# Performance work log

Measured on AMD Instinct MI355X. Metric: run time of the kernel, lower is better.

The kernel has to match this reference:

```python
import jax, jax.numpy as jnp
import numpy as np

DIM = 192; HEADS = 6; WS = 7; RES = 56; SHIFT = 3
HEAD_DIM = DIM // HEADS
SCALE = HEAD_DIM ** -0.5
N = WS * WS
EPS = 1e-5

def _rel_pos_index():
    coords = np.stack(np.meshgrid(np.arange(WS), np.arange(WS), indexing='ij')).reshape(2, -1)
    rel = coords[:, :, None] - coords[:, None, :]  # [2,N,N]
    rel = rel.transpose(1, 2, 0)
    rel[:, :, 0] += WS - 1
    rel[:, :, 1] += WS - 1
    rel[:, :, 0] *= 2 * WS - 1
    return rel.sum(-1)  # [N,N]

def _attn_mask():
    img = np.zeros((RES, RES), dtype=np.float32)
    slices = (slice(0, -WS), slice(-WS, -SHIFT), slice(-SHIFT, None))
    cnt = 0
    for h in slices:
        for w in slices:
            img[h, w] = cnt; cnt += 1
    mw = img.reshape(RES // WS, WS, RES // WS, WS).transpose(0, 2, 1, 3).reshape(-1, N)  # [nW,N]
    diff = mw[:, None, :] - mw[:, :, None]
    return np.where(diff != 0, -100.0, 0.0).astype(np.float32)  # [nW,N,N]

REL_IDX = jnp.asarray(_rel_pos_index())
ATTN_MASK = jnp.asarray(_attn_mask())

def _ln(x, g, b):
    mu = x.mean(-1, keepdims=True)
    var = ((x - mu) ** 2).mean(-1, keepdims=True)
    return (x - mu) * jax.lax.rsqrt(var + EPS) * g + b

def setup_inputs() -> dict:
    key = jax.random.key(0)
    ks = jax.random.split(key, 8)
    d = {
        'x': jax.random.normal(ks[0], (32, RES * RES, DIM), jnp.float32),
        'norm1_g': jnp.ones((DIM,), jnp.float32), 'norm1_b': jnp.zeros((DIM,), jnp.float32),
        'qkv_w': jax.random.normal(ks[1], (DIM, 3 * DIM), jnp.float32) * 0.02,
        'qkv_b': jnp.zeros((3 * DIM,), jnp.float32),
        'proj_w': jax.random.normal(ks[2], (DIM, DIM), jnp.float32) * 0.02,
        'proj_b': jnp.zeros((DIM,), jnp.float32),
        'bias_table': jax.random.normal(ks[3], ((2 * WS - 1) ** 2, HEADS), jnp.float32) * 0.02,
        'norm2_g': jnp.ones((DIM,), jnp.float32), 'norm2_b': jnp.zeros((DIM,), jnp.float32),
        'fc1_w': jax.random.normal(ks[4], (DIM, 4 * DIM), jnp.float32) * 0.02,
        'fc1_b': jnp.zeros((4 * DIM,), jnp.float32),
        'fc2_w': jax.random.normal(ks[5], (4 * DIM, DIM), jnp.float32) * 0.02,
        'fc2_b': jnp.zeros((DIM,), jnp.float32),
    }
    return d

def reference(x, norm1_g, norm1_b, qkv_w, qkv_b, proj_w, proj_b, bias_table,
              norm2_g, norm2_b, fc1_w, fc1_b, fc2_w, fc2_b):
    B, L, C = x.shape
    H = W = RES
    shortcut = x
    h = _ln(x, norm1_g, norm1_b).reshape(B, H, W, C)
    # cyclic shift
    h = jnp.roll(h, (-SHIFT, -SHIFT), axis=(1, 2))
    # window partition -> [B*nW, N, C]
    nH = H // WS
    h = h.reshape(B, nH, WS, nH, WS, C).transpose(0, 1, 3, 2, 4, 5).reshape(-1, N, C)
    BW = h.shape[0]
    # windowed MHSA
    qkv = (h @ qkv_w + qkv_b).reshape(BW, N, 3, HEADS, HEAD_DIM)
    q, k, v = qkv[:, :, 0], qkv[:, :, 1], qkv[:, :, 2]  # [BW,N,h,hd]
    attn = jnp.einsum('bnhd,bmhd->bhnm', q, k) * SCALE  # [BW,h,N,N]
    bias = bias_table[REL_IDX.reshape(-1)].reshape(N, N, HEADS).transpose(2, 0, 1)
    attn = attn + bias[None]
    nW = ATTN_MASK.shape[0]
    attn = attn.reshape(BW // nW, nW, HEADS, N, N) + ATTN_MASK[None, :, None]
    attn = jax.nn.softmax(attn.reshape(BW, HEADS, N, N), axis=-1)
    h = jnp.einsum('bhnm,bmhd->bnhd', attn, v).reshape(BW, N, C)
    h = h @ proj_w + proj_b
    # window reverse
    h = h.reshape(B, nH, nH, WS, WS, C).transpose(0, 1, 3, 2, 4, 5).reshape(B, H, W, C)
    h = jnp.roll(h, (SHIFT, SHIFT), axis=(1, 2)).reshape(B, L, C)
    x = shortcut + h
    # MLP
    m = _ln(x, norm2_g, norm2_b)
    m = jax.nn.gelu(m @ fc1_w + fc1_b, approximate=False) @ fc2_w + fc2_b
    return x + m
```

## Files before the change

kernel.cpp:

```cpp
#include <hip/hip_runtime.h>
#include <hip/hip_bf16.h>
#include <math.h>

typedef __attribute__((ext_vector_type(8))) short bh8;
typedef __attribute__((ext_vector_type(4))) short sh4;
typedef __attribute__((ext_vector_type(4))) float fx4;

__device__ __forceinline__ fx4 mfma_bf16(bh8 a, bh8 b, fx4 c) {
    return __builtin_amdgcn_mfma_f32_16x16x32_bf16(a, b, c, 0, 0, 0);
}

__device__ __forceinline__ void gload16(const __hip_bfloat16* g, __hip_bfloat16* l) {
    __builtin_amdgcn_global_load_lds(
        (const __attribute__((address_space(1))) void*)g,
        (__attribute__((address_space(3))) void*)l,
        16, 0, 0);
}

__device__ __forceinline__ float fast_erf(float u) {
    float au = fabsf(u);
    float t  = __builtin_amdgcn_rcpf(1.0f + 0.3275911f * au);
    float p  = ((((1.061405429f * t - 1.453152027f) * t + 1.421413741f) * t
                 - 0.284496736f) * t + 0.254829592f) * t;
    float e  = __expf(-u * u);
    return copysignf(1.0f - p * e, u);
}

#define WAITV6 do { asm volatile("s_waitcnt vmcnt(6)" ::: "memory"); \
                    __builtin_amdgcn_sched_barrier(0); } while (0)
#define WAITV0 do { asm volatile("s_waitcnt vmcnt(0)" ::: "memory"); \
                    __builtin_amdgcn_sched_barrier(0); } while (0)
#define LGKM0  do { asm volatile("s_waitcnt lgkmcnt(0)" ::: "memory"); \
                    __builtin_amdgcn_sched_barrier(0); } while (0)
#define BARR   do { __builtin_amdgcn_s_barrier(); \
                    __builtin_amdgcn_sched_barrier(0); } while (0)

__global__ __launch_bounds__(256)
void convw_all_k(const float* __restrict__ qkv_w, const float* __restrict__ proj_w,
                 const float* __restrict__ fc1_w, const float* __restrict__ fc2_w,
                 __hip_bfloat16* __restrict__ wq, __hip_bfloat16* __restrict__ wp,
                 __hip_bfloat16* __restrict__ w1, __hip_bfloat16* __restrict__ w2)
{
    int idx = blockIdx.x * 256 + threadIdx.x;
    if (idx < 110592) {
        int k = idx / 576, n = idx - k * 576;
        wq[(size_t)n * 192 + k] = __float2bfloat16(qkv_w[idx]);
        return;
    }
    idx -= 110592;
    if (idx < 36864) {
        int k = idx / 192, n = idx - k * 192;
        wp[(size_t)n * 192 + k] = __float2bfloat16(proj_w[idx]);
        return;
    }
    idx -= 36864;
    if (idx < 147456) {
        int k = idx / 768, n = idx - k * 768;
        w1[(size_t)n * 192 + k] = __float2bfloat16(fc1_w[idx]);
        return;
    }
    idx -= 147456;
    if (idx < 147456) {
        int k = idx / 192, n = idx - k * 192;
        w2[(size_t)n * 768 + k] = __float2bfloat16(fc2_w[idx]);
    }
}

__global__ __launch_bounds__(256)
void ln1_gather_k(const float* __restrict__ x, const float* __restrict__ g,
                  const float* __restrict__ bia, __hip_bfloat16* __restrict__ xw)
{
    const int wave = threadIdx.x >> 6, lane = threadIdx.x & 63;
    const int t = blockIdx.x * 4 + wave;
    const int w = t / 49, n = t - w * 49;
    const int b = w >> 6, wrem = w & 63, wi = wrem >> 3, wj = wrem & 7;
    const int i = n / 7, j = n - i * 7;
    int sr = wi * 7 + i + 3; if (sr >= 56) sr -= 56;
    int sc = wj * 7 + j + 3; if (sc >= 56) sc -= 56;
    const float* xp = x + ((size_t)b * 3136 + sr * 56 + sc) * 192;
    float v0 = xp[lane], v1 = xp[lane + 64], v2 = xp[lane + 128];
    float s = v0 + v1 + v2;
    float q = v0 * v0 + v1 * v1 + v2 * v2;
    for (int off = 32; off > 0; off >>= 1) {
        s += __shfl_down(s, off, 64);
        q += __shfl_down(q, off, 64);
    }
    s = __shfl(s, 0, 64); q = __shfl(q, 0, 64);
    float mean = s * (1.0f / 192.0f);
    float var  = q * (1.0f / 192.0f) - mean * mean;
    float rstd = rsqrtf(var + 1e-5f);
    __hip_bfloat16* op = xw + (size_t)t * 192;
    op[lane]       = __float2bfloat16((v0 - mean) * rstd * g[lane]       + bia[lane]);
    op[lane + 64]  = __float2bfloat16((v1 - mean) * rstd * g[lane + 64]  + bia[lane + 64]);
    op[lane + 128] = __float2bfloat16((v2 - mean) * rstd * g[lane + 128] + bia[lane + 128]);
}

template<int K, int NOUT>
__global__ __launch_bounds__(256)
void gemm_qkv_k(const __hip_bfloat16* __restrict__ A,
                const __hip_bfloat16* __restrict__ Bt,
                const float* __restrict__ bias,
                __hip_bfloat16* __restrict__ outv)
{
    __shared__ __align__(16) __hip_bfloat16 As[128 * 32];
    __shared__ __align__(16) __hip_bfloat16 Bs[64 * 32];
    const int tid  = threadIdx.x;
    const int lane = tid & 63, wave = tid >> 6;
    const int quad = lane >> 4, l15 = lane & 15;

    const int nb = NOUT / 64;
    const int wk = (blockIdx.x & 7) * ((int)gridDim.x >> 3) + ((int)blockIdx.x >> 3);
    const int m0 = (wk / nb) * 128, n0 = (wk % nb) * 64;

    const int arow = lane >> 2, acol = (lane & 3) * 8;
    const __hip_bfloat16* Ag0 = A  + (size_t)(m0 + wave * 32 + arow)      * K + acol;
    const __hip_bfloat16* Ag1 = A  + (size_t)(m0 + wave * 32 + 16 + arow) * K + acol;
    const __hip_bfloat16* Bg  = Bt + (size_t)(n0 + wave * 16 + arow)      * K + acol;
    __hip_bfloat16* Al0 = &As[(wave * 32)      * 32];
    __hip_bfloat16* Al1 = &As[(wave * 32 + 16) * 32];
    __hip_bfloat16* Bl  = &Bs[(wave * 16)      * 32];

    fx4 acc[2][4];
#pragma unroll
    for (int mi = 0; mi < 2; mi++)
#pragma unroll
        for (int ni = 0; ni < 4; ni++) acc[mi][ni] = {0.f, 0.f, 0.f, 0.f};

    for (int k0 = 0; k0 < K; k0 += 32) {
        gload16(Ag0 + k0, Al0);
        gload16(Ag1 + k0, Al1);
        gload16(Bg  + k0, Bl);
        __syncthreads();
        bh8 a0 = *(const bh8*)&As[(wave * 32 + l15)      * 32 + quad * 8];
        bh8 a1 = *(const bh8*)&As[(wave * 32 + 16 + l15) * 32 + quad * 8];
        bh8 b0 = *(const bh8*)&Bs[(0 * 16 + l15) * 32 + quad * 8];
        bh8 b1 = *(const bh8*)&Bs[(1 * 16 + l15) * 32 + quad * 8];
        bh8 b2 = *(const bh8*)&Bs[(2 * 16 + l15) * 32 + quad * 8];
        bh8 b3 = *(const bh8*)&Bs[(3 * 16 + l15) * 32 + quad * 8];
        acc[0][0] = mfma_bf16(a0, b0, acc[0][0]);
        acc[0][1] = mfma_bf16(a0, b1, acc[0][1]);
        acc[0][2] = mfma_bf16(a0, b2, acc[0][2]);
        acc[0][3] = mfma_bf16(a0, b3, acc[0][3]);
        acc[1][0] = mfma_bf16(a1, b0, acc[1][0]);
        acc[1][1] = mfma_bf16(a1, b1, acc[1][1]);
        acc[1][2] = mfma_bf16(a1, b2, acc[1][2]);
        acc[1][3] = mfma_bf16(a1, b3, acc[1][3]);
        __syncthreads();
    }

#pragma unroll
    for (int mi = 0; mi < 2; mi++)
#pragma unroll
    for (int ni = 0; ni < 4; ni++) {
        const int n = n0 + ni * 16 + l15;
        const float bn = bias[n];
#pragma unroll
        for (int r = 0; r < 4; r++) {
            const int m = m0 + wave * 32 + mi * 16 + quad * 4 + r;
            float v = acc[mi][ni][r] + bn;
            if (n < 192) v *= 0.17677669529663687f;
            outv[(size_t)m * NOUT + n] = __float2bfloat16(v);
        }
    }
}

__global__ __launch_bounds__(256, 2)
void mlp_k(const __hip_bfloat16* __restrict__ A,
           const __hip_bfloat16* __restrict__ W1t,
           const __hip_bfloat16* __restrict__ W2t,
           const float* __restrict__ b1,
           const float* __restrict__ b2,
           float* __restrict__ out)
{
    __shared__ __align__(16) __hip_bfloat16 W1s[2][6][32][32];
    __shared__ __align__(16) __hip_bfloat16 W2s[2][192][32];
    __shared__ __align__(16) __hip_bfloat16 Hs[128][40];
    __shared__ __align__(16) float b1s[768];

    const int tid  = threadIdx.x;
    const int lane = tid & 63, wave = tid >> 6;
    const int quad = lane >> 4, l15 = lane & 15;
    const int m0 = blockIdx.x * 128;
    const int arow = lane >> 2, acol = (lane & 3) * 8;

    if (tid < 192) ((fx4*)b1s)[tid] = ((const fx4*)b1)[tid];
    LGKM0;

    bh8 xr[2][6];
    const __hip_bfloat16* xg = A + (size_t)(m0 + wave * 32 + l15) * 192 + quad * 8;
#pragma unroll
    for (int rt = 0; rt < 2; rt++)
#pragma unroll
        for (int kc = 0; kc < 6; kc++)
            xr[rt][kc] = *(const bh8*)(xg + rt * 16 * 192 + kc * 32);

    auto stage = [&](int bf, int c) {
#pragma unroll
        for (int i = 0; i < 3; i++) {
            const int g = wave * 3 + i;
            const int kc = g >> 1, half = g & 1;
            gload16(W1t + (size_t)(c * 32 + half * 16 + arow) * 192 + kc * 32 + acol,
                    &W1s[bf][kc][half * 16][0]);
            gload16(W2t + (size_t)(g * 16 + arow) * 768 + c * 32 + acol,
                    &W2s[bf][g * 16][0]);
        }
    };

    fx4 acc2[2][12];
#pragma unroll
    for (int rt = 0; rt < 2; rt++)
#pragma unroll
        for (int nt = 0; nt < 12; nt++) acc2[rt][nt] = {0.f, 0.f, 0.f, 0.f};

    stage(0, 0);
    stage(1, 1);

    int cur = 0;
    for (int c = 0; c < 23; ++c) {
        WAITV6;
        BARR;

        fx4 bv0 = *(const fx4*)&b1s[c * 32 + quad * 4];
        fx4 bv1 = *(const fx4*)&b1s[c * 32 + 16 + quad * 4];

        fx4 acc1[2][2];
        acc1[0][0] = {0.f, 0.f, 0.f, 0.f}; acc1[0][1] = {0.f, 0.f, 0.f, 0.f};
        acc1[1][0] = {0.f, 0.f, 0.f, 0.f}; acc1[1][1] = {0.f, 0.f, 0.f, 0.f};
        __builtin_amdgcn_s_setprio(1);
#pragma unroll
        for (int kc = 0; kc < 6; kc++) {
#pragma unroll
            for (int ni = 0; ni < 2; ni++) {
                bh8 w = *(const bh8*)&W1s[cur][kc][ni * 16 + l15][quad * 8];
                acc1[0][ni] = mfma_bf16(w, xr[0][kc], acc1[0][ni]);
                acc1[1][ni] = mfma_bf16(w, xr[1][kc], acc1[1][ni]);
            }
        }
        __builtin_amdgcn_s_setprio(0);

#pragma unroll
        for (int rt = 0; rt < 2; rt++) {
#pragma unroll
            for (int ni = 0; ni < 2; ni++) {
                const fx4 bv = ni ? bv1 : bv0;
                sh4 pk;
#pragma unroll
                for (int r = 0; r < 4; r++) {
                    float v = acc1[rt][ni][r] + bv[r];
                    float h = 0.5f * v * (1.0f + fast_erf(v * 0.70710678118654752f));
                    union { __hip_bfloat16 hb; short s; } u;
                    u.hb = __float2bfloat16(h);
                    pk[r] = u.s;
                }
                *(sh4*)&Hs[wave * 32 + rt * 16 + l15][ni * 16 + quad * 4] = pk;
            }
        }
        LGKM0;

        bh8 ha0 = *(const bh8*)&Hs[wave * 32 + l15][quad * 8];
        bh8 ha1 = *(const bh8*)&Hs[wave * 32 + 16 + l15][quad * 8];
        __builtin_amdgcn_s_setprio(1);
#pragma unroll
        for (int nt = 0; nt < 12; nt++) {
            bh8 w2 = *(const bh8*)&W2s[cur][nt * 16 + l15][quad * 8];
            acc2[0][nt] = mfma_bf16(ha0, w2, acc2[0][nt]);
            acc2[1][nt] = mfma_bf16(ha1, w2, acc2[1][nt]);
        }
        __builtin_amdgcn_s_setprio(0);

        BARR;
        if (c < 22) stage(cur, c + 2);
        cur ^= 1;
    }

    {
        WAITV0;
        BARR;
        fx4 bv0 = *(const fx4*)&b1s[23 * 32 + 0 * 16 + quad * 4];
        fx4 bv1 = *(const fx4*)&b1s[23 * 32 + 1 * 16 + quad * 4];
        fx4 acc1[2][2];
        acc1[0][0] = {0.f, 0.f, 0.f, 0.f}; acc1[0][1] = {0.f, 0.f, 0.f, 0.f};
        acc1[1][0] = {0.f, 0.f, 0.f, 0.f}; acc1[1][1] = {0.f, 0.f, 0.f, 0.f};
#pragma unroll
        for (int kc = 0; kc < 6; kc++) {
#pragma unroll
            for (int ni = 0; ni < 2; ni++) {
                bh8 w = *(const bh8*)&W1s[cur][kc][ni * 16 + l15][quad * 8];
                acc1[0][ni] = mfma_bf16(w, xr[0][kc], acc1[0][ni]);
                acc1[1][ni] = mfma_bf16(w, xr[1][kc], acc1[1][ni]);
            }
        }
#pragma unroll
        for (int rt = 0; rt < 2; rt++) {
#pragma unroll
            for (int ni = 0; ni < 2; ni++) {
                const fx4 bv = ni ? bv1 : bv0;
                sh4 pk;
#pragma unroll
                for (int r = 0; r < 4; r++) {
                    float v = acc1[rt][ni][r] + bv[r];
                    float h = 0.5f * v * (1.0f + fast_erf(v * 0.70710678118654752f));
                    union { __hip_bfloat16 hb; short s; } u;
                    u.hb = __float2bfloat16(h);
                    pk[r] = u.s;
                }
                *(sh4*)&Hs[wave * 32 + rt * 16 + l15][ni * 16 + quad * 4] = pk;
            }
        }
        LGKM0;
        bh8 ha0 = *(const bh8*)&Hs[wave * 32 + l15][quad * 8];
        bh8 ha1 = *(const bh8*)&Hs[wave * 32 + 16 + l15][quad * 8];
#pragma unroll
        for (int nt = 0; nt < 12; nt++) {
            bh8 w2 = *(const bh8*)&W2s[cur][nt * 16 + l15][quad * 8];
            acc2[0][nt] = mfma_bf16(ha0, w2, acc2[0][nt]);
            acc2[1][nt] = mfma_bf16(ha1, w2, acc2[1][nt]);
        }
    }

#pragma unroll
    for (int rt = 0; rt < 2; rt++)
#pragma unroll
    for (int nt = 0; nt < 12; nt++) {
        const int n = nt * 16 + l15;
        const float bn = b2[n];
#pragma unroll
        for (int r = 0; r < 4; r++) {
            const int m = m0 + wave * 32 + rt * 16 + quad * 4 + r;
            out[(size_t)m * 192 + n] += acc2[rt][nt][r] + bn;
        }
    }
}

__global__ __launch_bounds__(256)
void projln_k(const __hip_bfloat16* __restrict__ A,
              const __hip_bfloat16* __restrict__ Bt,
              const float* __restrict__ pb,
              const float* __restrict__ xresid,
              const float* __restrict__ g2,
              const float* __restrict__ b2,
              float* __restrict__ x1out,
              __hip_bfloat16* __restrict__ y2out)
{
    __shared__ __align__(16) __hip_bfloat16 As[64 * 32];
    __shared__ __align__(16) __hip_bfloat16 Bs[192 * 32];
    const int tid  = threadIdx.x;
    const int lane = tid & 63, wave = tid >> 6;
    const int quad = lane >> 4, l15 = lane & 15;
    const int m0 = blockIdx.x * 64;

    const int arow = lane >> 2, acol = (lane & 3) * 8;
    const __hip_bfloat16* Ag = A + (size_t)(m0 + wave * 16 + arow) * 192 + acol;
    __hip_bfloat16* Al = &As[(wave * 16) * 32];
    const __hip_bfloat16* Bg0 = Bt + (size_t)((wave + 0) * 16 + arow) * 192 + acol;
    const __hip_bfloat16* Bg1 = Bt + (size_t)((wave + 4) * 16 + arow) * 192 + acol;
    const __hip_bfloat16* Bg2 = Bt + (size_t)((wave + 8) * 16 + arow) * 192 + acol;
    __hip_bfloat16* Bl0 = &Bs[((wave + 0) * 16) * 32];
    __hip_bfloat16* Bl1 = &Bs[((wave + 4) * 16) * 32];
    __hip_bfloat16* Bl2 = &Bs[((wave + 8) * 16) * 32];

    fx4 acc[12];
#pragma unroll
    for (int ct = 0; ct < 12; ct++) acc[ct] = {0.f, 0.f, 0.f, 0.f};

    for (int k0 = 0; k0 < 192; k0 += 32) {
        gload16(Ag  + k0, Al);
        gload16(Bg0 + k0, Bl0);
        gload16(Bg1 + k0, Bl1);
        gload16(Bg2 + k0, Bl2);
        __syncthreads();
        bh8 a = *(const bh8*)&As[(wave * 16 + l15) * 32 + quad * 8];
#pragma unroll
        for (int ct = 0; ct < 12; ct++) {
            bh8 b = *(const bh8*)&Bs[(ct * 16 + l15) * 32 + quad * 8];
            acc[ct] = mfma_bf16(a, b, acc[ct]);
        }
        __syncthreads();
    }

#pragma unroll
    for (int r = 0; r < 4; r++) {
        const int row = m0 + wave * 16 + quad * 4 + r;
        float vv[12];
        float s = 0.f, q = 0.f;
#pragma unroll
        for (int ct = 0; ct < 12; ct++) {
            const int col = ct * 16 + l15;
            float v = acc[ct][r] + pb[col] + xresid[(size_t)row * 192 + col];
            vv[ct] = v;
            x1out[(size_t)row * 192 + col] = v;
            s += v;
            q += v * v;
        }
        s += __shfl_xor(s, 1, 64);  q += __shfl_xor(q, 1, 64);
        s += __shfl_xor(s, 2, 64);  q += __shfl_xor(q, 2, 64);
        s += __shfl_xor(s, 4, 64);  q += __shfl_xor(q, 4, 64);
        s += __shfl_xor(s, 8, 64);  q += __shfl_xor(q, 8, 64);
        float mean = s * (1.0f / 192.0f);
        float var  = q * (1.0f / 192.0f) - mean * mean;
        float rstd = rsqrtf(var + 1e-5f);
#pragma unroll
        for (int ct = 0; ct < 12; ct++) {
            const int col = ct * 16 + l15;
            float y = (vv[ct] - mean) * rstd * g2[col] + b2[col];
            y2out[(size_t)row * 192 + col] = __float2bfloat16(y);
        }
    }
}

__global__ __launch_bounds__(256)
void attn_k(const __hip_bfloat16* __restrict__ qkv,
            const float* __restrict__ bias_table,
            __hip_bfloat16* __restrict__ aout)
{
    __shared__ __align__(16) __hip_bfloat16 Qb[64 * 32];
    __shared__ __align__(16) __hip_bfloat16 Kb[64 * 32];
    __shared__ __align__(16) __hip_bfloat16 Vt[32 * 72];
    __shared__ __align__(16) __hip_bfloat16 Ps[64 * 72];
    __shared__ float bias_h[169];

    const int tid  = threadIdx.x;
    const int lane = tid & 63, wave = tid >> 6;
    const int quad = lane >> 4, l15 = lane & 15;
    const int wk = (blockIdx.x & 7) * 1536 + ((int)blockIdx.x >> 3);
    const int w = wk / 6, hd = wk % 6;
    const int b = w >> 6, wrem = w & 63, wi = wrem >> 3, wj = wrem & 7;
    const size_t base = (size_t)w * 49 * 576 + hd * 32;

    if (tid < 169) bias_h[tid] = bias_table[tid * 6 + hd];

    bh8 z = {0, 0, 0, 0, 0, 0, 0, 0};
    {
        int row = tid >> 2, ch = (tid & 3) * 8;
        if (row < 49) {
            *(bh8*)&Qb[row * 32 + ch] = *(const bh8*)(qkv + base + (size_t)row * 576 + ch);
            *(bh8*)&Kb[row * 32 + ch] = *(const bh8*)(qkv + base + (size_t)row * 576 + 192 + ch);
        } else {
            *(bh8*)&Qb[row * 32 + ch] = z;
            *(bh8*)&Kb[row * 32 + ch] = z;
        }
        for (int i = tid; i < 288; i += 256)
            *(bh8*)&Vt[i * 8] = z;
    }
    __syncthreads();
    for (int idx = tid; idx < 49 * 32; idx += 256) {
        int n = idx >> 5, d = idx & 31;
        Vt[d * 72 + n] = qkv[base + (size_t)n * 576 + 384 + d];
    }
    __syncthreads();

    fx4 zf = {0.f, 0.f, 0.f, 0.f};
    bh8 aq = *(const bh8*)&Qb[(wave * 16 + l15) * 32 + quad * 8];
    fx4 sarr[4];
#pragma unroll
    for (int ni = 0; ni < 4; ni++) {
        bh8 bk = *(const bh8*)&Kb[(ni * 16 + l15) * 32 + quad * 8];
        sarr[ni] = mfma_bf16(aq, bk, zf);
    }

    int iarr[4], ria[4], cia[4], mbi[4];
#pragma unroll
    for (int r = 0; r < 4; r++) {
        int i = wave * 16 + quad * 4 + r;
        int ri = i / 7, ci = i - ri * 7;
        iarr[r] = i; ria[r] = ri; cia[r] = ci;
        int ar = wi * 7 + ri, ac = wj * 7 + ci;
        int br = (ar < 49) ? 0 : ((ar < 53) ? 1 : 2);
        int bc = (ac < 49) ? 0 : ((ac < 53) ? 1 : 2);
        mbi[r] = br * 3 + bc;
    }
    float vals[4][4];
#pragma unroll
    for (int ni = 0; ni < 4; ni++) {
        int jcol = ni * 16 + l15;
        int rj = jcol / 7, cj = jcol - rj * 7;
        int ar = wi * 7 + rj, ac = wj * 7 + cj;
        int br = (ar < 49) ? 0 : ((ar < 53) ? 1 : 2);
        int bc = (ac < 49) ? 0 : ((ac < 53) ? 1 : 2);
        int mbj = br * 3 + bc;
#pragma unroll
        for (int r = 0; r < 4; r++) {
            float v;
            if (jcol >= 49)            v = -1e30f;
            else if (iarr[r] >= 49)    v = 0.0f;
            else {
                int bidx = (ria[r] - rj + 6) * 13 + (cia[r] - cj + 6);
                v = sarr[ni][r] + bias_h[bidx] + ((mbi[r] != mbj) ? -100.0f : 0.0f);
            }
            vals[ni][r] = v;
        }
    }
#pragma unroll
    for (int r = 0; r < 4; r++) {
        float mx = fmaxf(fmaxf(vals[0][r], vals[1][r]), fmaxf(vals[2][r], vals[3][r]));
        mx = fmaxf(mx, __shfl_xor(mx, 1, 64));
        mx = fmaxf(mx, __shfl_xor(mx, 2, 64));
        mx = fmaxf(mx, __shfl_xor(mx, 4, 64));
        mx = fmaxf(mx, __shfl_xor(mx, 8, 64));
        float e0 = __expf(vals[0][r] - mx);
        float e1 = __expf(vals[1][r] - mx);
        float e2 = __expf(vals[2][r] - mx);
        float e3 = __expf(vals[3][r] - mx);
        float sm = e0 + e1 + e2 + e3;
        sm += __shfl_xor(sm, 1, 64);
        sm += __shfl_xor(sm, 2, 64);
        sm += __shfl_xor(sm, 4, 64);
        sm += __shfl_xor(sm, 8, 64);
        float inv = 1.0f / sm;
        int prow = (wave * 16 + quad * 4 + r) * 72;
        Ps[prow + 0 * 16 + l15] = __float2bfloat16(e0 * inv);
        Ps[prow + 1 * 16 + l15] = __float2bfloat16(e1 * inv);
        Ps[prow + 2 * 16 + l15] = __float2bfloat16(e2 * inv);
        Ps[prow + 3 * 16 + l15] = __float2bfloat16(e3 * inv);
    }
    __syncthreads();

    fx4 o0 = zf, o1 = zf;
#pragma unroll
    for (int k0 = 0; k0 < 64; k0 += 32) {
        bh8 ap  = *(const bh8*)&Ps[(wave * 16 + l15) * 72 + k0 + quad * 8];
        bh8 bv0 = *(const bh8*)&Vt[(l15)      * 72 + k0 + quad * 8];
        bh8 bv1 = *(const bh8*)&Vt[(16 + l15) * 72 + k0 + quad * 8];
        o0 = mfma_bf16(ap, bv0, o0);
        o1 = mfma_bf16(ap, bv1, o1);
    }

#pragma unroll
    for (int r = 0; r < 4; r++) {
        int m = wave * 16 + quad * 4 + r;
        if (m < 49) {
            int i = m / 7, j2 = m - i * 7;
            int orow = wi * 7 + i + 3;  if (orow >= 56) orow -= 56;
            int ocol = wj * 7 + j2 + 3; if (ocol >= 56) ocol -= 56;
            size_t t = (size_t)b * 3136 + orow * 56 + ocol;
            aout[t * 192 + hd * 32 + l15]      = __float2bfloat16(o0[r]);
            aout[t * 192 + hd * 32 + 16 + l15] = __float2bfloat16(o1[r]);
        }
    }
}

extern "C" void kernel_launch(void* const* d_in, const int* in_sizes, int n_in,
                              void* d_out, int out_size, void* d_ws, size_t ws_size,
                              hipStream_t stream)
{
    const float* x      = (const float*)d_in[0];
    const float* n1g    = (const float*)d_in[1];
    const float* n1b    = (const float*)d_in[2];
    const float* qkv_w  = (const float*)d_in[3];
    const float* qkv_b  = (const float*)d_in[4];
    const float* proj_w = (const float*)d_in[5];
    const float* proj_b = (const float*)d_in[6];
    const float* btab   = (const float*)d_in[7];
    const float* n2g    = (const float*)d_in[8];
    const float* n2b    = (const float*)d_in[9];
    const float* fc1_w  = (const float*)d_in[10];
    const float* fc1_b  = (const float*)d_in[11];
    const float* fc2_w  = (const float*)d_in[12];
    const float* fc2_b  = (const float*)d_in[13];

    char* ws = (char*)d_ws;
    __hip_bfloat16* buf1    = (__hip_bfloat16*)(ws + 0);
    __hip_bfloat16* buf2    = (__hip_bfloat16*)(ws + 38535168);
    __hip_bfloat16* wt_qkv  = (__hip_bfloat16*)(ws + 192675840);
    __hip_bfloat16* wt_proj = (__hip_bfloat16*)(ws + 192897024);
    __hip_bfloat16* wt_fc1  = (__hip_bfloat16*)(ws + 192970752);
    __hip_bfloat16* wt_fc2  = (__hip_bfloat16*)(ws + 193265664);
    float*          x1      = (float*)d_out;

    convw_all_k<<<dim3(1728), 256, 0, stream>>>(qkv_w, proj_w, fc1_w, fc2_w,
                                                wt_qkv, wt_proj, wt_fc1, wt_fc2);

    ln1_gather_k<<<dim3(25088), 256, 0, stream>>>(x, n1g, n1b, buf1);

    gemm_qkv_k<192, 576><<<dim3(7056), 256, 0, stream>>>(buf1, wt_qkv, qkv_b, buf2);

    attn_k<<<dim3(12288), 256, 0, stream>>>(buf2, btab, buf1);

    projln_k<<<dim3(1568), 256, 0, stream>>>(buf1, wt_proj, proj_b, x, n2g, n2b, x1, buf1);

    mlp_k<<<dim3(784), 256, 0, stream>>>(buf1, wt_fc1, wt_fc2, fc1_b, fc2_b, x1);
}
```

Before: 444.2 us.

## Fuse LayerNorm1 and window gather into the QKV GEMM kernel

Merges the LN1+shift/window-gather kernel with the QKV projection GEMM. Each block normalizes 64 tokens into LDS as bf16, then loops over all 9 output column tiles reusing that A tile. This removes the bf16 intermediate write/read of the normalized activations and one kernel launch. The cost is a smaller M tile per block and serialized N tiles with barriers, which may reduce parallelism and weight reuse per block.

```diff
diff --git a/kernel.cpp b/kernel.cpp
--- a/kernel.cpp
+++ b/kernel.cpp
@@ -24,6 +24,12 @@
                  - 0.284496736f) * t + 0.254829592f) * t;
     float e  = __expf(-u * u);
     return copysignf(1.0f - p * e, u);
+}
+
+__device__ __forceinline__ short bf16s(float f) {
+    union { __hip_bfloat16 h; short s; } u;
+    u.h = __float2bfloat16(f);
+    return u.s;
 }
 
 #define WAITV6 do { asm volatile("s_waitcnt vmcnt(6)" ::: "memory"); \
@@ -67,100 +73,97 @@
 }
 
 __global__ __launch_bounds__(256)
-void ln1_gather_k(const float* __restrict__ x, const float* __restrict__ g,
-                  const float* __restrict__ bia, __hip_bfloat16* __restrict__ xw)
+void lnqkv_k(const float* __restrict__ x, const float* __restrict__ g,
+             const float* __restrict__ bia,
+             const __hip_bfloat16* __restrict__ Bt,
+             const float* __restrict__ qb,
+             __hip_bfloat16* __restrict__ outv)
 {
-    const int wave = threadIdx.x >> 6, lane = threadIdx.x & 63;
-    const int t = blockIdx.x * 4 + wave;
-    const int w = t / 49, n = t - w * 49;
-    const int b = w >> 6, wrem = w & 63, wi = wrem >> 3, wj = wrem & 7;
-    const int i = n / 7, j = n - i * 7;
-    int sr = wi * 7 + i + 3; if (sr >= 56) sr -= 56;
-    int sc = wj * 7 + j + 3; if (sc >= 56) sc -= 56;
-    const float* xp = x + ((size_t)b * 3136 + sr * 56 + sc) * 192;
-    float v0 = xp[lane], v1 = xp[lane + 64], v2 = xp[lane + 128];
-    float s = v0 + v1 + v2;
-    float q = v0 * v0 + v1 * v1 + v2 * v2;
-    for (int off = 32; off > 0; off >>= 1) {
-        s += __shfl_down(s, off, 64);
-        q += __shfl_down(q, off, 64);
-    }
-    s = __shfl(s, 0, 64); q = __shfl(q, 0, 64);
-    float mean = s * (1.0f / 192.0f);
-    float var  = q * (1.0f / 192.0f) - mean * mean;
-    float rstd = rsqrtf(var + 1e-5f);
-    __hip_bfloat16* op = xw + (size_t)t * 192;
-    op[lane]       = __float2bfloat16((v0 - mean) * rstd * g[lane]       + bia[lane]);
-    op[lane + 64]  = __float2bfloat16((v1 - mean) * rstd * g[lane + 64]  + bia[lane + 64]);
-    op[lane + 128] = __float2bfloat16((v2 - mean) * rstd * g[lane + 128] + bia[lane + 128]);
-}
-
-template<int K, int NOUT>
-__global__ __launch_bounds__(256)
-void gemm_qkv_k(const __hip_bfloat16* __restrict__ A,
-                const __hip_bfloat16* __restrict__ Bt,
-                const float* __restrict__ bias,
-                __hip_bfloat16* __restrict__ outv)
-{
-    __shared__ __align__(16) __hip_bfloat16 As[128 * 32];
-    __shared__ __align__(16) __hip_bfloat16 Bs[64 * 32];
+    __shared__ __align__(16) __hip_bfloat16 Xs[6][64][32];
+    __shared__ __align__(16) __hip_bfloat16 Bs[6][64][32];
+
     const int tid  = threadIdx.x;
     const int lane = tid & 63, wave = tid >> 6;
     const int quad = lane >> 4, l15 = lane & 15;
-
-    const int nb = NOUT / 64;
-    const int wk = (blockIdx.x & 7) * ((int)gridDim.x >> 3) + ((int)blockIdx.x >> 3);
-    const int m0 = (wk / nb) * 128, n0 = (wk % nb) * 64;
-
+    const int m0 = blockIdx.x * 64;
     const int arow = lane >> 2, acol = (lane & 3) * 8;
-    const __hip_bfloat16* Ag0 = A  + (size_t)(m0 + wave * 32 + arow)      * K + acol;
-    const __hip_bfloat16* Ag1 = A  + (size_t)(m0 + wave * 32 + 16 + arow) * K + acol;
-    const __hip_bfloat16* Bg  = Bt + (size_t)(n0 + wave * 16 + arow)      * K + acol;
-    __hip_bfloat16* Al0 = &As[(wave * 32)      * 32];
-    __hip_bfloat16* Al1 = &As[(wave * 32 + 16) * 32];
-    __hip_bfloat16* Bl  = &Bs[(wave * 16)      * 32];
-
-    fx4 acc[2][4];
-#pragma unroll
-    for (int mi = 0; mi < 2; mi++)
-#pragma unroll
-        for (int ni = 0; ni < 4; ni++) acc[mi][ni] = {0.f, 0.f, 0.f, 0.f};
-
-    for (int k0 = 0; k0 < K; k0 += 32) {
-        gload16(Ag0 + k0, Al0);
-        gload16(Ag1 + k0, Al1);
-        gload16(Bg  + k0, Bl);
+
+    {
+        const int r = tid >> 2, c = tid & 3;
+        const int t = m0 + r;
+        const int w = t / 49, n = t - w * 49;
+        const int b = w >> 6, wrem = w & 63, wi = wrem >> 3, wj = wrem & 7;
+        const int i = n / 7, j = n - i * 7;
+        int sr = wi * 7 + i + 3; if (sr >= 56) sr -= 56;
+        int sc = wj * 7 + j + 3; if (sc >= 56) sc -= 56;
+        const float* xp = x + ((size_t)b * 3136 + sr * 56 + sc) * 192 + c * 48;
+
+        fx4 v[12];
+        float s = 0.f, q = 0.f;
+#pragma unroll
+        for (int u = 0; u < 12; u++) {
+            v[u] = *(const fx4*)(xp + u * 4);
+            s += v[u][0] + v[u][1] + v[u][2] + v[u][3];
+            q += v[u][0]*v[u][0] + v[u][1]*v[u][1] + v[u][2]*v[u][2] + v[u][3]*v[u][3];
+        }
+        s += __shfl_xor(s, 1, 64);  q += __shfl_xor(q, 1, 64);
+        s += __shfl_xor(s, 2, 64);  q += __shfl_xor(q, 2, 64);
+        float mean = s * (1.0f / 192.0f);
+        float var  = q * (1.0f / 192.0f) - mean * mean;
+        float rstd = rsqrtf(var + 1e-5f);
+
+#pragma unroll
+        for (int jj = 0; jj < 6; jj++) {
+            const int col = c * 48 + jj * 8;
+            const fx4 g0 = *(const fx4*)(g + col),     g1 = *(const fx4*)(g + col + 4);
+            const fx4 b0 = *(const fx4*)(bia + col),   b1 = *(const fx4*)(bia + col + 4);
+            union { short sh[8]; bh8 v8; } pk;
+#pragma unroll
+            for (int e = 0; e < 4; e++) {
+                const int f0 = jj * 8 + e, f1 = jj * 8 + 4 + e;
+                pk.sh[e]     = bf16s((v[f0 >> 2][f0 & 3] - mean) * rstd * g0[e] + b0[e]);
+                pk.sh[e + 4] = bf16s((v[f1 >> 2][f1 & 3] - mean) * rstd * g1[e] + b1[e]);
+            }
+            *(bh8*)&Xs[col >> 5][r][col & 31] = pk.v8;
+        }
+    }
+
+    for (int nb = 0; nb < 9; nb++) {
+#pragma unroll
+        for (int i2 = 0; i2 < 6; i2++) {
+            const int gi = wave * 6 + i2;
+            const int kc = gi >> 2, seg = gi & 3;
+            gload16(Bt + (size_t)(nb * 64 + seg * 16 + arow) * 192 + kc * 32 + acol,
+                    &Bs[kc][seg * 16][0]);
+        }
         __syncthreads();
-        bh8 a0 = *(const bh8*)&As[(wave * 32 + l15)      * 32 + quad * 8];
-        bh8 a1 = *(const bh8*)&As[(wave * 32 + 16 + l15) * 32 + quad * 8];
-        bh8 b0 = *(const bh8*)&Bs[(0 * 16 + l15) * 32 + quad * 8];
-        bh8 b1 = *(const bh8*)&Bs[(1 * 16 + l15) * 32 + quad * 8];
-        bh8 b2 = *(const bh8*)&Bs[(2 * 16 + l15) * 32 + quad * 8];
-        bh8 b3 = *(const bh8*)&Bs[(3 * 16 + l15) * 32 + quad * 8];
-        acc[0][0] = mfma_bf16(a0, b0, acc[0][0]);
-        acc[0][1] = mfma_bf16(a0, b1, acc[0][1]);
-        acc[0][2] = mfma_bf16(a0, b2, acc[0][2]);
-        acc[0][3] = mfma_bf16(a0, b3, acc[0][3]);
-        acc[1][0] = mfma_bf16(a1, b0, acc[1][0]);
-        acc[1][1] = mfma_bf16(a1, b1, acc[1][1]);
-        acc[1][2] = mfma_bf16(a1, b2, acc[1][2]);
-        acc[1][3] = mfma_bf16(a1, b3, acc[1][3]);
+
+        fx4 acc[4];
+#pragma unroll
+        for (int ni = 0; ni < 4; ni++) acc[ni] = {0.f, 0.f, 0.f, 0.f};
+#pragma unroll
+        for (int kc = 0; kc < 6; kc++) {
+            bh8 a = *(const bh8*)&Xs[kc][wave * 16 + l15][quad * 8];
+#pragma unroll
+            for (int ni = 0; ni < 4; ni++) {
+                bh8 bfrag = *(const bh8*)&Bs[kc][ni * 16 + l15][quad * 8];
+                acc[ni] = mfma_bf16(a, bfrag, acc[ni]);
+            }
+        }
+
+#pragma unroll
+        for (int ni = 0; ni < 4; ni++) {
+            const int n = nb * 64 + ni * 16 + l15;
+            const float bn = qb[n];
+#pragma unroll
+            for (int r = 0; r < 4; r++) {
+                const int m = m0 + wave * 16 + quad * 4 + r;
+                float val = acc[ni][r] + bn;
+                if (n < 192) val *= 0.17677669529663687f;
+                outv[(size_t)m * 576 + n] = __float2bfloat16(val);
+            }
+        }
         __syncthreads();
-    }
-
-#pragma unroll
-    for (int mi = 0; mi < 2; mi++)
-#pragma unroll
-    for (int ni = 0; ni < 4; ni++) {
-        const int n = n0 + ni * 16 + l15;
-        const float bn = bias[n];
-#pragma unroll
-        for (int r = 0; r < 4; r++) {
-            const int m = m0 + wave * 32 + mi * 16 + quad * 4 + r;
-            float v = acc[mi][ni][r] + bn;
-            if (n < 192) v *= 0.17677669529663687f;
-            outv[(size_t)m * NOUT + n] = __float2bfloat16(v);
-        }
     }
 }
 
@@ -248,9 +251,7 @@
                 for (int r = 0; r < 4; r++) {
                     float v = acc1[rt][ni][r] + bv[r];
                     float h = 0.5f * v * (1.0f + fast_erf(v * 0.70710678118654752f));
-                    union { __hip_bfloat16 hb; short s; } u;
-                    u.hb = __float2bfloat16(h);
-                    pk[r] = u.s;
+                    pk[r] = bf16s(h);
                 }
                 *(sh4*)&Hs[wave * 32 + rt * 16 + l15][ni * 16 + quad * 4] = pk;
             }
@@ -300,9 +301,7 @@
                 for (int r = 0; r < 4; r++) {
                     float v = acc1[rt][ni][r] + bv[r];
                     float h = 0.5f * v * (1.0f + fast_erf(v * 0.70710678118654752f));
-                    union { __hip_bfloat16 hb; short s; } u;
-                    u.hb = __float2bfloat16(h);
-                    pk[r] = u.s;
+                    pk[r] = bf16s(h);
                 }
                 *(sh4*)&Hs[wave * 32 + rt * 16 + l15][ni * 16 + quad * 4] = pk;
             }
@@ -570,9 +569,7 @@
     convw_all_k<<<dim3(1728), 256, 0, stream>>>(qkv_w, proj_w, fc1_w, fc2_w,
                                                 wt_qkv, wt_proj, wt_fc1, wt_fc2);
 
-    ln1_gather_k<<<dim3(25088), 256, 0, stream>>>(x, n1g, n1b, buf1);
-
-    gemm_qkv_k<192, 576><<<dim3(7056), 256, 0, stream>>>(buf1, wt_qkv, qkv_b, buf2);
+    lnqkv_k<<<dim3(1568), 256, 0, stream>>>(x, n1g, n1b, wt_qkv, qkv_b, buf2);
 
     attn_k<<<dim3(12288), 256, 0, stream>>>(buf2, btab, buf1);
 
```

Result: no change. 447.1 us (+0.6%).
